# Performance work log

Hardware: AMD Instinct MI355X
Metric: run time of the kernel (lower is better)

Reference implementation:

```python
import jax, jax.numpy as jnp
import numpy as np

EPS = 1e-8  # torch CosineSimilarity default eps

def setup_inputs() -> dict:
    key = jax.random.key(0)
    kv, kt, k1, k2, k3, k4 = jax.random.split(key, 6)
    B, S = 16, 1024
    VD, TD, H = 1024, 768, 512
    visual_features = jax.random.normal(kv, (B, S, VD), dtype=jnp.float32)
    text_features = jax.random.normal(kt, (B, S, TD), dtype=jnp.float32)
    # nn.Linear params: weight [out, in], bias [out]
    Wv = jax.random.normal(k1, (H, VD), dtype=jnp.float32) * (1.0 / np.sqrt(VD))
    bv = jax.random.normal(k2, (H,), dtype=jnp.float32) * 0.01
    Wt = jax.random.normal(k3, (H, TD), dtype=jnp.float32) * (1.0 / np.sqrt(TD))
    bt = jax.random.normal(k4, (H,), dtype=jnp.float32) * 0.01
    return {"visual_features": visual_features, "text_features": text_features,
            "Wv": Wv, "bv": bv, "Wt": Wt, "bt": bt}

def reference(visual_features, text_features, Wv, bv, Wt, bt):
    # Linear projections
    v = jnp.einsum('bsd,hd->bsh', visual_features, Wv) + bv  # [B,S,H]
    t = jnp.einsum('bsd,hd->bsh', text_features, Wt) + bt    # [B,S,H]
    # Cosine similarity matrix via normalized batched GEMM
    # (algebraically equal to broadcasting CosineSimilarity over (B,S,S,H))
    dots = jnp.einsum('bih,bjh->bij', v, t)                   # [B,S,S]
    vn = jnp.linalg.norm(v, axis=-1)                          # [B,S]
    tn = jnp.linalg.norm(t, axis=-1)                          # [B,S]
    denom = jnp.maximum(vn[:, :, None] * tn[:, None, :], EPS)
    return dots / denom
```

## Files before the change

### kernel.cpp

```cpp
#include <hip/hip_runtime.h>
#include <hip/hip_bf16.h>

typedef __bf16 bf16x8 __attribute__((ext_vector_type(8)));
typedef __bf16 bf16x4 __attribute__((ext_vector_type(4)));
typedef float  f32x4  __attribute__((ext_vector_type(4)));

#define MFMA16(a, b, c) __builtin_amdgcn_mfma_f32_16x16x32_bf16((a), (b), (c), 0, 0, 0)

#define BATCH 16
#define SEQ   1024
#define VD    1024
#define TD    768
#define HDIM  512
#define MROWS (BATCH * SEQ)

typedef __attribute__((address_space(1))) const unsigned int gas_uint;
typedef __attribute__((address_space(3))) unsigned int las_uint;

__device__ __forceinline__ void async_copy16(const void* g, void* l) {
    __builtin_amdgcn_global_load_lds((gas_uint*)g, (las_uint*)l, 16, 0, 0);
}

__device__ __forceinline__ void stage_tile_bf16(const __bf16* __restrict__ src,
                                                size_t ld, int row0, int k0,
                                                __bf16* __restrict__ buf, int tid) {
#pragma unroll
    for (int i = 0; i < 4; ++i) {
        const int c = i * 256 + tid;
        const int r = c >> 3;
        const int g = (c & 7) ^ (r & 7);
        async_copy16(&src[(size_t)(row0 + r) * ld + k0 + g * 8],
                     &buf[(c & ~63) * 8]);
    }
}

__device__ __forceinline__ bf16x8 frag_read(const __bf16* __restrict__ buf,
                                            int r, int h, int fq) {
    return *reinterpret_cast<const bf16x8*>(&buf[(r * 8 + ((h * 4 + fq) ^ (r & 7))) * 8]);
}

#define NC_XV (BATCH * SEQ * VD / 4)
#define NC_XT (BATCH * SEQ * TD / 4)
#define NC_WV (HDIM * VD / 4)
#define NC_WT (HDIM * TD / 4)
#define NC_TOTAL (NC_XV + NC_XT + NC_WV + NC_WT)

__global__ __launch_bounds__(256) void conv_kernel(
    const float* __restrict__ Xv, const float* __restrict__ Xt,
    const float* __restrict__ Wv, const float* __restrict__ Wt,
    __bf16* __restrict__ Xvb, __bf16* __restrict__ Xtb,
    __bf16* __restrict__ Wvb, __bf16* __restrict__ Wtb) {
    int i = blockIdx.x * 256 + threadIdx.x;
    if (i >= NC_TOTAL) return;
    const float* src;
    __bf16* dst;
    if (i < NC_XV)                     { src = Xv; dst = Xvb; }
    else if ((i -= NC_XV) < NC_XT)     { src = Xt; dst = Xtb; }
    else if ((i -= NC_XT) < NC_WV)     { src = Wv; dst = Wvb; }
    else { i -= NC_WV;                   src = Wt; dst = Wtb; }
    const float4 x = reinterpret_cast<const float4*>(src)[i];
    bf16x4 p = {(__bf16)x.x, (__bf16)x.y, (__bf16)x.z, (__bf16)x.w};
    reinterpret_cast<bf16x4*>(dst)[i] = p;
}

__global__ __launch_bounds__(256) void proj_kernel(
    const __bf16* __restrict__ Xvb, const __bf16* __restrict__ Wvb, const float* __restrict__ bv_,
    const __bf16* __restrict__ Xtb, const __bf16* __restrict__ Wtb, const float* __restrict__ bt_,
    __bf16* __restrict__ vout, __bf16* __restrict__ tout,
    float* __restrict__ vn2, float* __restrict__ tn2)
{
    const int L     = blockIdx.x;
    const int mlow  = L & 7;
    const int n     = (L >> 3) & 3;
    const int mhigh = (L >> 5) & 15;
    const int z     = L >> 9;
    const int m0    = (mhigh * 8 + mlow) * 128;
    const int n0    = n * 128;

    const __bf16* X; const __bf16* Wb; const float* bias; __bf16* out; float* n2; int K;
    if (z == 0) { X = Xvb; Wb = Wvb; bias = bv_; out = vout; n2 = vn2; K = VD; }
    else        { X = Xtb; Wb = Wtb; bias = bt_; out = tout; n2 = tn2; K = TD; }

    __shared__ __bf16 As[2][128 * 64];
    __shared__ __bf16 Bs[2][128 * 64];

    const int tid  = threadIdx.x;
    const int lane = tid & 63;
    const int wave = tid >> 6;
    const int wr   = wave >> 1;
    const int wc   = wave & 1;
    const int fr   = lane & 15;
    const int fq   = lane >> 4;

    f32x4 acc[4][4] = {};
    const int nk = K >> 6;

    stage_tile_bf16(X,  K, m0, 0, As[0], tid);
    stage_tile_bf16(Wb, K, n0, 0, Bs[0], tid);
    __syncthreads();

    for (int ki = 0; ki < nk; ++ki) {
        if (ki + 1 < nk) {
            const int kk = (ki + 1) << 6;
            stage_tile_bf16(X,  K, m0, kk, As[(ki + 1) & 1], tid);
            stage_tile_bf16(Wb, K, n0, kk, Bs[(ki + 1) & 1], tid);
        }
        const __bf16* Ab = As[ki & 1];
        const __bf16* Bb = Bs[ki & 1];
#pragma unroll
        for (int h = 0; h < 2; ++h) {
            bf16x8 a[4], b[4];
#pragma unroll
            for (int tm = 0; tm < 4; ++tm)
                a[tm] = frag_read(Ab, wr * 64 + tm * 16 + fr, h, fq);
#pragma unroll
            for (int tn = 0; tn < 4; ++tn)
                b[tn] = frag_read(Bb, wc * 64 + tn * 16 + fr, h, fq);
#pragma unroll
            for (int tm = 0; tm < 4; ++tm)
#pragma unroll
                for (int tn = 0; tn < 4; ++tn)
                    acc[tm][tn] = MFMA16(a[tm], b[tn], acc[tm][tn]);
        }
        __syncthreads();
    }

    float bc[4];
#pragma unroll
    for (int tn = 0; tn < 4; ++tn)
        bc[tn] = bias[n0 + wc * 64 + tn * 16 + fr];

#pragma unroll
    for (int tm = 0; tm < 4; ++tm) {
        const int rowb = m0 + wr * 64 + tm * 16 + fq * 4;
#pragma unroll
        for (int r = 0; r < 4; ++r) {
            float s = 0.f;
#pragma unroll
            for (int tn = 0; tn < 4; ++tn) {
                const float e = acc[tm][tn][r] + bc[tn];
                out[(size_t)(rowb + r) * HDIM + n0 + wc * 64 + tn * 16 + fr] = (__bf16)e;
                s = fmaf(e, e, s);
            }
            s += __shfl_xor(s, 1);
            s += __shfl_xor(s, 2);
            s += __shfl_xor(s, 4);
            s += __shfl_xor(s, 8);
            if (fr == 0) atomicAdd(&n2[rowb + r], s);
        }
    }
}

__global__ __launch_bounds__(256) void dots_kernel(const __bf16* __restrict__ v,
                                                   const __bf16* __restrict__ t,
                                                   const float* __restrict__ vn2,
                                                   const float* __restrict__ tn2,
                                                   float* __restrict__ out) {
    __shared__ __bf16 As[2][128 * 64];
    __shared__ __bf16 Bs[2][128 * 64];

    const int L  = blockIdx.x;
    const int b  = (L & 7) + ((L >> 9) << 3);
    const int j0 = ((L >> 3) & 7) * 128;
    const int i0 = ((L >> 6) & 7) * 128;

    const __bf16* vb = v + (size_t)b * SEQ * HDIM;
    const __bf16* tb = t + (size_t)b * SEQ * HDIM;

    const int tid  = threadIdx.x;
    const int lane = tid & 63;
    const int wave = tid >> 6;
    const int wr   = wave >> 1;
    const int wc   = wave & 1;
    const int fr   = lane & 15;
    const int fq   = lane >> 4;

    f32x4 acc[4][4] = {};
    const int nk = HDIM >> 6;

    stage_tile_bf16(vb, HDIM, i0, 0, As[0], tid);
    stage_tile_bf16(tb, HDIM, j0, 0, Bs[0], tid);
    __syncthreads();

    for (int ki = 0; ki < nk; ++ki) {
        if (ki + 1 < nk) {
            const int kk = (ki + 1) << 6;
            stage_tile_bf16(vb, HDIM, i0, kk, As[(ki + 1) & 1], tid);
            stage_tile_bf16(tb, HDIM, j0, kk, Bs[(ki + 1) & 1], tid);
        }
        const __bf16* Ab = As[ki & 1];
        const __bf16* Bb = Bs[ki & 1];
#pragma unroll
        for (int h = 0; h < 2; ++h) {
            bf16x8 a[4], bfr[4];
#pragma unroll
            for (int tm = 0; tm < 4; ++tm)
                a[tm] = frag_read(Ab, wr * 64 + tm * 16 + fr, h, fq);
#pragma unroll
            for (int tn = 0; tn < 4; ++tn)
                bfr[tn] = frag_read(Bb, wc * 64 + tn * 16 + fr, h, fq);
#pragma unroll
            for (int tm = 0; tm < 4; ++tm)
#pragma unroll
                for (int tn = 0; tn < 4; ++tn)
                    acc[tm][tn] = MFMA16(a[tm], bfr[tn], acc[tm][tn]);
        }
        __syncthreads();
    }

    float vr2[16];
#pragma unroll
    for (int tm = 0; tm < 4; ++tm)
#pragma unroll
        for (int r = 0; r < 4; ++r)
            vr2[tm * 4 + r] = vn2[b * SEQ + i0 + wr * 64 + tm * 16 + fq * 4 + r];

    float* outb = out + ((size_t)b << 20);
#pragma unroll
    for (int tn = 0; tn < 4; ++tn) {
        const int j     = j0 + wc * 64 + tn * 16 + fr;
        const float tj2 = tn2[b * SEQ + j];
#pragma unroll
        for (int tm = 0; tm < 4; ++tm) {
            const int ib = i0 + wr * 64 + tm * 16 + fq * 4;
#pragma unroll
            for (int r = 0; r < 4; ++r) {
                const float denom = fmaxf(sqrtf(vr2[tm * 4 + r] * tj2), 1e-8f);
                outb[(size_t)(ib + r) * SEQ + j] = acc[tm][tn][r] * __builtin_amdgcn_rcpf(denom);
            }
        }
    }
}

extern "C" void kernel_launch(void* const* d_in, const int* in_sizes, int n_in,
                              void* d_out, int out_size, void* d_ws, size_t ws_size,
                              hipStream_t stream) {
    const float* Xv = (const float*)d_in[0];
    const float* Xt = (const float*)d_in[1];
    const float* Wv = (const float*)d_in[2];
    const float* bv = (const float*)d_in[3];
    const float* Wt = (const float*)d_in[4];
    const float* bt = (const float*)d_in[5];
    float* out = (float*)d_out;

    char* ws = (char*)d_ws;
    size_t off = 0;
    __bf16* v   = (__bf16*)(ws + off); off += (size_t)MROWS * HDIM * 2;
    __bf16* t   = (__bf16*)(ws + off); off += (size_t)MROWS * HDIM * 2;
    __bf16* Xvb = (__bf16*)(ws + off); off += (size_t)MROWS * VD * 2;
    __bf16* Xtb = (__bf16*)(ws + off); off += (size_t)MROWS * TD * 2;
    __bf16* Wvb = (__bf16*)(ws + off); off += (size_t)HDIM * VD * 2;
    __bf16* Wtb = (__bf16*)(ws + off); off += (size_t)HDIM * TD * 2;
    float*  vn2 = (float*)(ws + off);  off += (size_t)MROWS * 4;
    float*  tn2 = (float*)(ws + off);  off += (size_t)MROWS * 4;

    hipMemsetAsync(vn2, 0, (size_t)2 * MROWS * 4, stream);

    conv_kernel<<<(NC_TOTAL + 255) / 256, 256, 0, stream>>>(Xv, Xt, Wv, Wt, Xvb, Xtb, Wvb, Wtb);

    proj_kernel<<<1024, 256, 0, stream>>>(Xvb, Wvb, bv, Xtb, Wtb, bt, v, t, vn2, tn2);

    dots_kernel<<<1024, 256, 0, stream>>>(v, t, vn2, tn2, out);
}
```

Before: 248.8 us.

## Enlarge dots GEMM tile to 256x256 with 8 waves and deeper prefetch

The batched dots kernel now uses 256x256 output tiles computed by 512 threads (8 waves, 2x4 layout), with two k-tiles staged ahead through async LDS loads and explicit vmcnt waits. The MFMA phase is interleaved with barriers and priority raises, and the block-to-batch mapping is changed. Larger tiles cut global reloads of v/t per output element and should hide load latency better. The cost is 128KB of LDS, more registers per thread, and only 256 blocks, which may leave some CUs idle.

```diff
diff --git a/kernel.cpp b/kernel.cpp
--- a/kernel.cpp
+++ b/kernel.cpp
@@ -27,6 +27,19 @@
 #pragma unroll
     for (int i = 0; i < 4; ++i) {
         const int c = i * 256 + tid;
+        const int r = c >> 3;
+        const int g = (c & 7) ^ (r & 7);
+        async_copy16(&src[(size_t)(row0 + r) * ld + k0 + g * 8],
+                     &buf[(c & ~63) * 8]);
+    }
+}
+
+__device__ __forceinline__ void stage_tile256(const __bf16* __restrict__ src,
+                                              size_t ld, int row0, int k0,
+                                              __bf16* __restrict__ buf, int tid) {
+#pragma unroll
+    for (int i = 0; i < 4; ++i) {
+        const int c = i * 512 + tid;
         const int r = c >> 3;
         const int g = (c & 7) ^ (r & 7);
         async_copy16(&src[(size_t)(row0 + r) * ld + k0 + g * 8],
@@ -151,18 +164,20 @@
     }
 }
 
-__global__ __launch_bounds__(256) void dots_kernel(const __bf16* __restrict__ v,
-                                                   const __bf16* __restrict__ t,
-                                                   const float* __restrict__ vn2,
-                                                   const float* __restrict__ tn2,
-                                                   float* __restrict__ out) {
-    __shared__ __bf16 As[2][128 * 64];
-    __shared__ __bf16 Bs[2][128 * 64];
+__global__ __launch_bounds__(512, 2) void dots_kernel(const __bf16* __restrict__ v,
+                                                      const __bf16* __restrict__ t,
+                                                      const float* __restrict__ vn2,
+                                                      const float* __restrict__ tn2,
+                                                      float* __restrict__ out) {
+    __shared__ __bf16 As[2][256 * 64];
+    __shared__ __bf16 Bs[2][256 * 64];
 
     const int L  = blockIdx.x;
-    const int b  = (L & 7) + ((L >> 9) << 3);
-    const int j0 = ((L >> 3) & 7) * 128;
-    const int i0 = ((L >> 6) & 7) * 128;
+    const int x  = L & 7;
+    const int s  = L >> 3;
+    const int b  = x * 2 + (s >> 4);
+    const int i0 = ((s >> 2) & 3) * 256;
+    const int j0 = (s & 3) * 256;
 
     const __bf16* vb = v + (size_t)b * SEQ * HDIM;
     const __bf16* tb = t + (size_t)b * SEQ * HDIM;
@@ -170,63 +185,86 @@
     const int tid  = threadIdx.x;
     const int lane = tid & 63;
     const int wave = tid >> 6;
-    const int wr   = wave >> 1;
-    const int wc   = wave & 1;
+    const int wr   = wave >> 2;
+    const int wc   = wave & 3;
     const int fr   = lane & 15;
     const int fq   = lane >> 4;
 
-    f32x4 acc[4][4] = {};
-    const int nk = HDIM >> 6;
-
-    stage_tile_bf16(vb, HDIM, i0, 0, As[0], tid);
-    stage_tile_bf16(tb, HDIM, j0, 0, Bs[0], tid);
-    __syncthreads();
-
-    for (int ki = 0; ki < nk; ++ki) {
-        if (ki + 1 < nk) {
-            const int kk = (ki + 1) << 6;
-            stage_tile_bf16(vb, HDIM, i0, kk, As[(ki + 1) & 1], tid);
-            stage_tile_bf16(tb, HDIM, j0, kk, Bs[(ki + 1) & 1], tid);
-        }
-        const __bf16* Ab = As[ki & 1];
-        const __bf16* Bb = Bs[ki & 1];
-#pragma unroll
-        for (int h = 0; h < 2; ++h) {
-            bf16x8 a[4], bfr[4];
-#pragma unroll
-            for (int tm = 0; tm < 4; ++tm)
-                a[tm] = frag_read(Ab, wr * 64 + tm * 16 + fr, h, fq);
-#pragma unroll
-            for (int tn = 0; tn < 4; ++tn)
-                bfr[tn] = frag_read(Bb, wc * 64 + tn * 16 + fr, h, fq);
-#pragma unroll
-            for (int tm = 0; tm < 4; ++tm)
-#pragma unroll
-                for (int tn = 0; tn < 4; ++tn)
-                    acc[tm][tn] = MFMA16(a[tm], bfr[tn], acc[tm][tn]);
-        }
-        __syncthreads();
-    }
-
-    float vr2[16];
-#pragma unroll
-    for (int tm = 0; tm < 4; ++tm)
+    f32x4 acc[8][4] = {};
+    const int NKT = HDIM >> 6;
+
+    stage_tile256(vb, HDIM, i0, 0,  As[0], tid);
+    stage_tile256(tb, HDIM, j0, 0,  Bs[0], tid);
+    stage_tile256(vb, HDIM, i0, 64, As[1], tid);
+    stage_tile256(tb, HDIM, j0, 64, Bs[1], tid);
+    asm volatile("s_waitcnt vmcnt(8)" ::: "memory");
+    __builtin_amdgcn_s_barrier();
+
+    for (int kt = 0; kt < NKT; ++kt) {
+        const __bf16* Ab = As[kt & 1];
+        const __bf16* Bb = Bs[kt & 1];
+        bf16x8 bfr[4][2];
+#pragma unroll
+        for (int q = 0; q < 4; ++q) {
+            bf16x8 afr[2][2];
+#pragma unroll
+            for (int m2 = 0; m2 < 2; ++m2)
+#pragma unroll
+                for (int h = 0; h < 2; ++h)
+                    afr[m2][h] = frag_read(Ab, wr * 128 + (q * 2 + m2) * 16 + fr, h, fq);
+            if (q == 0) {
+#pragma unroll
+                for (int n = 0; n < 4; ++n)
+#pragma unroll
+                    for (int h = 0; h < 2; ++h)
+                        bfr[n][h] = frag_read(Bb, wc * 64 + n * 16 + fr, h, fq);
+            }
+            __builtin_amdgcn_s_barrier();
+            __builtin_amdgcn_s_setprio(1);
+#pragma unroll
+            for (int h = 0; h < 2; ++h)
+#pragma unroll
+                for (int m2 = 0; m2 < 2; ++m2)
+#pragma unroll
+                    for (int n = 0; n < 4; ++n)
+                        acc[q * 2 + m2][n] = MFMA16(afr[m2][h], bfr[n][h], acc[q * 2 + m2][n]);
+            __builtin_amdgcn_s_setprio(0);
+        }
+        if (kt < NKT - 1) {
+            __builtin_amdgcn_s_barrier();
+            __builtin_amdgcn_sched_barrier(0);
+            if (kt + 2 < NKT) {
+                const int kk = (kt + 2) << 6;
+                stage_tile256(vb, HDIM, i0, kk, As[kt & 1], tid);
+                stage_tile256(tb, HDIM, j0, kk, Bs[kt & 1], tid);
+                asm volatile("s_waitcnt vmcnt(8)" ::: "memory");
+            } else {
+                asm volatile("s_waitcnt vmcnt(0)" ::: "memory");
+            }
+            __builtin_amdgcn_sched_barrier(0);
+            __builtin_amdgcn_s_barrier();
+        }
+    }
+
+    float vr2[8][4];
+#pragma unroll
+    for (int mf = 0; mf < 8; ++mf)
 #pragma unroll
         for (int r = 0; r < 4; ++r)
-            vr2[tm * 4 + r] = vn2[b * SEQ + i0 + wr * 64 + tm * 16 + fq * 4 + r];
+            vr2[mf][r] = vn2[b * SEQ + i0 + wr * 128 + mf * 16 + fq * 4 + r];
 
     float* outb = out + ((size_t)b << 20);
 #pragma unroll
-    for (int tn = 0; tn < 4; ++tn) {
-        const int j     = j0 + wc * 64 + tn * 16 + fr;
+    for (int n = 0; n < 4; ++n) {
+        const int j     = j0 + wc * 64 + n * 16 + fr;
         const float tj2 = tn2[b * SEQ + j];
 #pragma unroll
-        for (int tm = 0; tm < 4; ++tm) {
-            const int ib = i0 + wr * 64 + tm * 16 + fq * 4;
+        for (int mf = 0; mf < 8; ++mf) {
+            const int ib = i0 + wr * 128 + mf * 16 + fq * 4;
 #pragma unroll
             for (int r = 0; r < 4; ++r) {
-                const float denom = fmaxf(sqrtf(vr2[tm * 4 + r] * tj2), 1e-8f);
-                outb[(size_t)(ib + r) * SEQ + j] = acc[tm][tn][r] * __builtin_amdgcn_rcpf(denom);
+                const float denom = fmaxf(sqrtf(vr2[mf][r] * tj2), 1e-8f);
+                outb[(size_t)(ib + r) * SEQ + j] = acc[mf][n][r] * __builtin_amdgcn_rcpf(denom);
             }
         }
     }
@@ -260,5 +298,5 @@
 
     proj_kernel<<<1024, 256, 0, stream>>>(Xvb, Wvb, bv, Xtb, Wtb, bt, v, t, vn2, tn2);
 
-    dots_kernel<<<1024, 256, 0, stream>>>(v, t, vn2, tn2, out);
-}
+    dots_kernel<<<256, 512, 0, stream>>>(v, t, vn2, tn2, out);
+}
```

Result: faster. 236.9 us (-4.8%).
